# Optimization experiments

Measured on AMD Instinct MI355X. Metric: run time of the kernel, lower is better.

The kernel has to match this reference:

```python
import jax, jax.numpy as jnp
import numpy as np
import math

B, SQ, SK = 8, 1024, 1024
DQ = DK = DV = 1024
H = 16
EPS = 1e-5


def _layer_norm(x, g, b):
    mu = jnp.mean(x, axis=-1, keepdims=True)
    var = jnp.mean(jnp.square(x - mu), axis=-1, keepdims=True)
    return (x - mu) * jax.lax.rsqrt(var + EPS) * g + b


def setup_inputs() -> dict:
    key = jax.random.key(0)
    ks = jax.random.split(key, 8)
    s_q = 1.0 / math.sqrt(DQ)
    s_v = 1.0 / math.sqrt(DV)
    return {
        "Q": jax.random.normal(ks[0], (B, SQ, DQ), dtype=jnp.float32),
        "K": jax.random.normal(ks[1], (B, SK, DK), dtype=jnp.float32),
        "Wq": jax.random.normal(ks[2], (DQ, DV), dtype=jnp.float32) * s_q,
        "bq": jnp.zeros((DV,), dtype=jnp.float32),
        "Wk": jax.random.normal(ks[3], (DK, DV), dtype=jnp.float32) * s_q,
        "bk": jnp.zeros((DV,), dtype=jnp.float32),
        "Wv": jax.random.normal(ks[4], (DK, DV), dtype=jnp.float32) * s_q,
        "bv": jnp.zeros((DV,), dtype=jnp.float32),
        "Wo": jax.random.normal(ks[5], (DV, DV), dtype=jnp.float32) * s_v,
        "bo": jnp.zeros((DV,), dtype=jnp.float32),
        "g0": jnp.ones((DV,), dtype=jnp.float32),
        "b0": jnp.zeros((DV,), dtype=jnp.float32),
        "g1": jnp.ones((DV,), dtype=jnp.float32),
        "b1": jnp.zeros((DV,), dtype=jnp.float32),
    }


def reference(Q, K, Wq, bq, Wk, bk, Wv, bv, Wo, bo, g0, b0, g1, b1):
    dh = DV // H
    q = Q @ Wq + bq                      # [B,SQ,DV]
    k = K @ Wk + bk                      # [B,SK,DV]
    v = K @ Wv + bv                      # [B,SK,DV]
    # split/cat over heads == reshape to [B,S,H,dh]
    qh = q.reshape(B, SQ, H, dh)
    kh = k.reshape(B, SK, H, dh)
    vh = v.reshape(B, SK, H, dh)
    # NOTE: original scales by sqrt(dim_V), not sqrt(head_dim)
    scores = jnp.einsum("bqhd,bkhd->bhqk", qh, kh) / math.sqrt(DV)
    A = jax.nn.softmax(scores, axis=-1)  # [B,H,SQ,SK]
    attn = jnp.einsum("bhqk,bkhd->bqhd", A, vh)
    out = q + attn.reshape(B, SQ, DV)    # residual with projected Q
    out = _layer_norm(out, g0, b0)
    out = out + jax.nn.relu(out @ Wo + bo)
    out = _layer_norm(out, g1, b1)
    return out
```

## Files before the change

kernel.cpp:

```cpp
#include <hip/hip_runtime.h>
#include <hip/hip_bf16.h>
#include <stdint.h>

#define NB 8
#define NSQ 1024
#define NSK 1024
#define ND 1024
#define NH 16
#define NDH 64
#define NM (NB * NSQ)
#define LOG2E 1.4426950408889634f

typedef __bf16 bf16;
typedef __bf16 bf16x8 __attribute__((ext_vector_type(8)));
typedef float f32x4 __attribute__((ext_vector_type(4)));
typedef float f32x16 __attribute__((ext_vector_type(16)));
typedef unsigned int uint32;

__device__ __forceinline__ void async_load16(const void* g, void* l) {
  __builtin_amdgcn_global_load_lds(
      (__attribute__((address_space(1))) void*)g,
      (__attribute__((address_space(3))) void*)l, 16, 0, 0);
}

__device__ __forceinline__ void permswap(uint32& x, uint32& y) {
#if __has_builtin(__builtin_amdgcn_permlane32_swap)
  auto r = __builtin_amdgcn_permlane32_swap(x, y, false, false);
  x = r[0]; y = r[1];
#else
  asm volatile("v_permlane32_swap_b32 %0, %1" : "+v"(x), "+v"(y));
#endif
}

__global__ __launch_bounds__(256) void cvt2_f32_bf16(const float* __restrict__ A,
                                                     const float* __restrict__ B,
                                                     bf16* __restrict__ Oa,
                                                     bf16* __restrict__ Ob) {
  const float* in = blockIdx.y ? B : A;
  bf16* out = blockIdx.y ? Ob : Oa;
  int i = blockIdx.x * 256 + threadIdx.x;
  float4 v = *(const float4*)(in + (size_t)i * 4);
  union { uint64_t u; bf16 h[4]; } o;
  o.h[0] = (bf16)v.x; o.h[1] = (bf16)v.y; o.h[2] = (bf16)v.z; o.h[3] = (bf16)v.w;
  *(uint64_t*)(out + (size_t)i * 4) = o.u;
}

__global__ __launch_bounds__(256) void transpose_cvt4(
    const float* __restrict__ W0, const float* __restrict__ W1,
    const float* __restrict__ W2, const float* __restrict__ W3,
    bf16* __restrict__ O0, bf16* __restrict__ O1,
    bf16* __restrict__ O2, bf16* __restrict__ O3) {
  const float* W; bf16* Wt;
  switch (blockIdx.z) {
    case 0: W = W0; Wt = O0; break;
    case 1: W = W1; Wt = O1; break;
    case 2: W = W2; Wt = O2; break;
    default: W = W3; Wt = O3; break;
  }
  __shared__ float t[64][65];
  const int bc = blockIdx.x * 64;
  const int br = blockIdx.y * 64;
  const int tid = threadIdx.x;
  for (int c = tid; c < 1024; c += 256) {
    int r = c >> 4, off = (c & 15) * 4;
    float4 v = *(const float4*)&W[(size_t)(br + r) * 1024 + bc + off];
    t[r][off] = v.x; t[r][off + 1] = v.y; t[r][off + 2] = v.z; t[r][off + 3] = v.w;
  }
  __syncthreads();
  for (int c = tid; c < 512; c += 256) {
    int cc = c >> 3, rr = (c & 7) * 8;
    union { uint4 u; bf16 h[8]; } o;
#pragma unroll
    for (int i = 0; i < 8; ++i) o.h[i] = (bf16)t[rr + i][cc];
    *(uint4*)&Wt[(size_t)(bc + cc) * 1024 + br + rr] = o.u;
  }
}

__global__ __launch_bounds__(256) void transpose_v(const bf16* __restrict__ vsrc,
                                                   bf16* __restrict__ vT) {
  const int st = blockIdx.x * 64;
  const int bh = blockIdx.y;
  const int b = bh >> 4, h = bh & 15;
  __shared__ __align__(16) bf16 t[64][72];
  const int tid = threadIdx.x;
  for (int c = tid; c < 512; c += 256) {
    int s = c >> 3, off = (c & 7) * 8;
    *(uint4*)&t[s][off] =
        *(const uint4*)&vsrc[(size_t)(b * NSK + st + s) * 2048 + 1024 + h * NDH + off];
  }
  __syncthreads();
  for (int c = tid; c < 512; c += 256) {
    int d = c >> 3, s0 = (c & 7) * 8;
    union { uint4 u; bf16 h[8]; } o;
#pragma unroll
    for (int i = 0; i < 8; ++i) o.h[i] = t[s0 + i][d];
    *(uint4*)&vT[((size_t)(bh * NDH + d)) * NSK + st + s0] = o.u;
  }
}

template <int BM, int MODE, int NX>
__global__ __launch_bounds__(512, 2) void gemm8p(
    const bf16* __restrict__ A, const bf16* __restrict__ Bt,
    const float* __restrict__ bias, const float* __restrict__ bias2,
    bf16* __restrict__ Cb, const bf16* __restrict__ Resb, float scale, int N) {
  constexpr int RA = BM / 64;
  constexpr int NT = 16;
  constexpr int MR = BM / 32;
  __shared__ __align__(16) bf16 As[2][BM * 64];
  __shared__ __align__(16) bf16 Bs[2][256 * 64];

  const int tid = threadIdx.x;
  const int flat = blockIdx.x;
  const int nwg = gridDim.x;
  const int xi = (flat & 7) * (nwg >> 3) + (flat >> 3);
  const int bcol = (xi & (NX - 1)) * 256;
  const int brow = (xi / NX) * BM;

  const int w = tid >> 6, lane = tid & 63;
  const int wm = w >> 2, wn = w & 3;
  const int lr = lane & 15, l4 = lane >> 4;
  const int rgrp = l4 * 4;
  const int rk = lr & 7;

  const int rowoff = tid >> 3;
  const int gsrc = (tid & 7) ^ ((tid >> 3) & 7);
  const bf16* Ag = A + (size_t)(brow + rowoff) * 1024 + gsrc * 8;
  const bf16* Bg = Bt + (size_t)(bcol + rowoff) * 1024 + gsrc * 8;
  const int lds_o = rowoff * 64 + (tid & 7) * 8;

  auto stA = [&](int d, int r, int kt) {
    async_load16(Ag + (size_t)r * (64 * 1024) + kt * 64, &As[d][r * 4096 + lds_o]);
  };
  auto stB = [&](int d, int r, int kt) {
    async_load16(Bg + (size_t)r * (64 * 1024) + kt * 64, &Bs[d][r * 4096 + lds_o]);
  };
  auto fA = [&](int d, int mrow, int ks) {
    return *(const bf16x8*)&As[d][(mrow + lr) * 64 + (((ks * 4 + l4) ^ rk) * 8)];
  };
  auto fB = [&](int d, int nrow, int ks) {
    return *(const bf16x8*)&Bs[d][(nrow + lr) * 64 + (((ks * 4 + l4) ^ rk) * 8)];
  };

  f32x4 acc[MR][4] = {};
  bf16x8 af[4][2], bfr[4][2];

#pragma unroll
  for (int r = 0; r < RA; ++r) stA(0, r, 0);
#pragma unroll
  for (int r = 0; r < 4; ++r) stB(0, r, 0);
  stA(1, 0, 1);
  stA(1, 1, 1);
  asm volatile("s_waitcnt vmcnt(2)" ::: "memory");
  __builtin_amdgcn_s_barrier();

  for (int t = 0; t < NT; ++t) {
    const int cur = t & 1, nxt = cur ^ 1;
#pragma unroll
    for (int i = 0; i < 4; ++i) {
      af[i][0] = fA(cur, wm * (BM / 2) + i * 16, 0);
      af[i][1] = fA(cur, wm * (BM / 2) + i * 16, 1);
    }
#pragma unroll
    for (int j = 0; j < 2; ++j) {
      bfr[j][0] = fB(cur, wn * 64 + j * 16, 0);
      bfr[j][1] = fB(cur, wn * 64 + j * 16, 1);
    }
    if (t + 1 < NT) {
      if constexpr (BM == 256) { stA(nxt, 2, t + 1); stA(nxt, 3, t + 1); }
      else                     { stB(nxt, 0, t + 1); stB(nxt, 1, t + 1); }
    }
    __builtin_amdgcn_s_barrier();
    asm volatile("s_waitcnt lgkmcnt(0)" ::: "memory");
    __builtin_amdgcn_sched_barrier(0);
    __builtin_amdgcn_s_setprio(1);
    if constexpr (BM == 256) {
#pragma unroll
      for (int i = 0; i < 4; ++i)
#pragma unroll
        for (int j = 0; j < 2; ++j)
#pragma unroll
          for (int ks = 0; ks < 2; ++ks)
            acc[i][j] = __builtin_amdgcn_mfma_f32_16x16x32_bf16(af[i][ks], bfr[j][ks], acc[i][j], 0, 0, 0);
    } else {
#pragma unroll
      for (int i = 0; i < 4; ++i)
#pragma unroll
        for (int ks = 0; ks < 2; ++ks)
          acc[i][0] = __builtin_amdgcn_mfma_f32_16x16x32_bf16(af[i][ks], bfr[0][ks], acc[i][0], 0, 0, 0);
    }
    __builtin_amdgcn_s_setprio(0);
    __builtin_amdgcn_s_barrier();
#pragma unroll
    for (int j = 2; j < 4; ++j) {
      bfr[j][0] = fB(cur, wn * 64 + j * 16, 0);
      bfr[j][1] = fB(cur, wn * 64 + j * 16, 1);
    }
    if (t + 1 < NT) {
      if constexpr (BM == 256) { stB(nxt, 0, t + 1); stB(nxt, 1, t + 1); }
      else                     { stB(nxt, 2, t + 1); stB(nxt, 3, t + 1); }
    }
    __builtin_amdgcn_s_barrier();
    asm volatile("s_waitcnt lgkmcnt(0)" ::: "memory");
    __builtin_amdgcn_sched_barrier(0);
    __builtin_amdgcn_s_setprio(1);
    if constexpr (BM == 256) {
#pragma unroll
      for (int i = 0; i < 4; ++i)
#pragma unroll
        for (int j = 2; j < 4; ++j)
#pragma unroll
          for (int ks = 0; ks < 2; ++ks)
            acc[i][j] = __builtin_amdgcn_mfma_f32_16x16x32_bf16(af[i][ks], bfr[j][ks], acc[i][j], 0, 0, 0);
    } else {
#pragma unroll
      for (int i = 0; i < 4; ++i)
#pragma unroll
        for (int ks = 0; ks < 2; ++ks)
          acc[i][1] = __builtin_amdgcn_mfma_f32_16x16x32_bf16(af[i][ks], bfr[1][ks], acc[i][1], 0, 0, 0);
    }
    __builtin_amdgcn_s_setprio(0);
    __builtin_amdgcn_s_barrier();
    if constexpr (BM == 256) {
#pragma unroll
      for (int i = 0; i < 4; ++i) {
        af[i][0] = fA(cur, wm * 128 + 64 + i * 16, 0);
        af[i][1] = fA(cur, wm * 128 + 64 + i * 16, 1);
      }
      if (t + 1 < NT) { stB(nxt, 2, t + 1); stB(nxt, 3, t + 1); }
    }
    __builtin_amdgcn_s_barrier();
    if constexpr (BM == 256) {
      asm volatile("s_waitcnt lgkmcnt(0)" ::: "memory");
      __builtin_amdgcn_sched_barrier(0);
    }
    __builtin_amdgcn_s_setprio(1);
    if constexpr (BM == 256) {
#pragma unroll
      for (int i = 0; i < 4; ++i)
#pragma unroll
        for (int j = 0; j < 2; ++j)
#pragma unroll
          for (int ks = 0; ks < 2; ++ks)
            acc[4 + i][j] = __builtin_amdgcn_mfma_f32_16x16x32_bf16(af[i][ks], bfr[j][ks], acc[4 + i][j], 0, 0, 0);
    } else {
#pragma unroll
      for (int i = 0; i < 4; ++i)
#pragma unroll
        for (int ks = 0; ks < 2; ++ks)
          acc[i][2] = __builtin_amdgcn_mfma_f32_16x16x32_bf16(af[i][ks], bfr[2][ks], acc[i][2], 0, 0, 0);
    }
    __builtin_amdgcn_s_setprio(0);
    __builtin_amdgcn_s_barrier();
    if (t + 2 < NT) { stA(cur, 0, t + 2); stA(cur, 1, t + 2); }
    __builtin_amdgcn_s_barrier();
    __builtin_amdgcn_s_setprio(1);
    if constexpr (BM == 256) {
#pragma unroll
      for (int i = 0; i < 4; ++i)
#pragma unroll
        for (int j = 2; j < 4; ++j)
#pragma unroll
          for (int ks = 0; ks < 2; ++ks)
            acc[4 + i][j] = __builtin_amdgcn_mfma_f32_16x16x32_bf16(af[i][ks], bfr[j][ks], acc[4 + i][j], 0, 0, 0);
    } else {
#pragma unroll
      for (int i = 0; i < 4; ++i)
#pragma unroll
        for (int ks = 0; ks < 2; ++ks)
          acc[i][3] = __builtin_amdgcn_mfma_f32_16x16x32_bf16(af[i][ks], bfr[3][ks], acc[i][3], 0, 0, 0);
    }
    __builtin_amdgcn_s_setprio(0);
    if (t + 1 < NT) {
      if (t + 2 < NT) asm volatile("s_waitcnt vmcnt(2)" ::: "memory");
      else            asm volatile("s_waitcnt vmcnt(0)" ::: "memory");
    }
    __builtin_amdgcn_s_barrier();
  }

#pragma unroll
  for (int m = 0; m < MR; ++m) {
#pragma unroll
    for (int n = 0; n < 4; ++n) {
      const int col = bcol + wn * 64 + n * 16 + lr;
      float bv, sc;
      if (MODE == 2) {
        const bool isV = (bcol >= 1024);
        bv = isV ? bias2[col - 1024] : bias[col];
        sc = isV ? 1.0f : LOG2E;
      } else {
        bv = bias[col];
        sc = scale;
      }
#pragma unroll
      for (int r = 0; r < 4; ++r) {
        const int row = brow + wm * (BM / 2) + m * 16 + rgrp + r;
        float v = acc[m][n][r] + bv;
        if (MODE == 1) {
          float res = (float)Resb[(size_t)row * N + col];
          Cb[(size_t)row * N + col] = (bf16)(res + (v > 0.f ? v : 0.f));
        } else {
          Cb[(size_t)row * N + col] = (bf16)(v * sc);
        }
      }
    }
  }
}

__global__ __launch_bounds__(512, 4) void attn_kernel(
    const bf16* __restrict__ qb, const bf16* __restrict__ kvb,
    const bf16* __restrict__ vT, bf16* __restrict__ attnout) {
  const int bh = blockIdx.y;
  const int b = bh >> 4, h = bh & 15;
  const int tid = threadIdx.x, w = tid >> 6, lane = tid & 63;
  const int l31 = lane & 31;
  const int l1 = lane >> 5;
  const int q0w = blockIdx.x * 256 + w * 32;

  __shared__ __align__(16) bf16 Kl[2][64 * 64];
  __shared__ __align__(16) bf16 Vl[2][64 * 64];

  const int srow = tid >> 3;
  const int sgran = tid & 7;
  const int gsw = sgran ^ (srow & 7);
  const int ldst = srow * 64 + sgran * 8;
  const int rg = l31 & 7;

  const bf16* kbase = kvb + (size_t)(b * NSK) * 2048 + h * NDH;
  const bf16* vbase = vT + (size_t)(bh * NDH) * NSK;

  bf16x8 qf[4];
#pragma unroll
  for (int kd = 0; kd < 4; ++kd)
    qf[kd] = *(const bf16x8*)&qb[(size_t)(b * NSQ + q0w + l31) * ND +
                                 h * NDH + kd * 16 + l1 * 8];

  f32x16 oacc0 = {}, oacc1 = {}, lacc = {};
  bf16x8 ones;
#pragma unroll
  for (int i = 0; i < 8; ++i) ones[i] = (bf16)1.0f;

  auto stage = [&](int bi, int kt) {
    async_load16(kbase + (size_t)(kt + srow) * 2048 + gsw * 8, &Kl[bi][ldst]);
    async_load16(vbase + (size_t)srow * NSK + kt + gsw * 8, &Vl[bi][ldst]);
  };

  stage(0, 0);

  for (int t = 0; t < 16; ++t) {
    const int bi = t & 1;
    asm volatile("s_waitcnt vmcnt(0)" ::: "memory");
    __syncthreads();
    if (t < 15) stage(bi ^ 1, (t + 1) * 64);

    uint32 W[2][4][2];
#pragma unroll
    for (int n = 0; n < 2; ++n) {
      f32x16 s = {};
      __builtin_amdgcn_s_setprio(1);
#pragma unroll
      for (int kd = 0; kd < 4; ++kd) {
        bf16x8 kf = *(const bf16x8*)&Kl[bi][(n * 32 + l31) * 64 + (((kd * 2 + l1) ^ rg) * 8)];
        s = __builtin_amdgcn_mfma_f32_32x32x16_bf16(kf, qf[kd], s, 0, 0, 0);
      }
      __builtin_amdgcn_s_setprio(0);
#pragma unroll
      for (int r2 = 0; r2 < 4; ++r2)
#pragma unroll
        for (int p = 0; p < 2; ++p) {
          float elo = __builtin_amdgcn_exp2f(s[r2 * 4 + 2 * p]);
          float ehi = __builtin_amdgcn_exp2f(s[r2 * 4 + 2 * p + 1]);
          uint32 wd;
          asm("v_cvt_pk_bf16_f32 %0, %1, %2" : "=v"(wd) : "v"(elo), "v"(ehi));
          W[n][r2][p] = wd;
        }
    }
    __builtin_amdgcn_s_setprio(1);
#pragma unroll
    for (int kc = 0; kc < 4; ++kc) {
      uint32 x0 = W[kc >> 1][(kc & 1) * 2][0], y0 = W[kc >> 1][(kc & 1) * 2 + 1][0];
      uint32 x1 = W[kc >> 1][(kc & 1) * 2][1], y1 = W[kc >> 1][(kc & 1) * 2 + 1][1];
      permswap(x0, y0);
      permswap(x1, y1);
      union { uint32 u[4]; bf16x8 v; } cvt;
      cvt.u[0] = x0; cvt.u[1] = x1; cvt.u[2] = y0; cvt.u[3] = y1;
      bf16x8 pa = cvt.v;
      bf16x8 vf0 = *(const bf16x8*)&Vl[bi][(l31) * 64 + (((kc * 2 + l1) ^ rg) * 8)];
      bf16x8 vf1 = *(const bf16x8*)&Vl[bi][(32 + l31) * 64 + (((kc * 2 + l1) ^ rg) * 8)];
      oacc0 = __builtin_amdgcn_mfma_f32_32x32x16_bf16(pa, vf0, oacc0, 0, 0, 0);
      oacc1 = __builtin_amdgcn_mfma_f32_32x32x16_bf16(pa, vf1, oacc1, 0, 0, 0);
      lacc = __builtin_amdgcn_mfma_f32_32x32x16_bf16(pa, ones, lacc, 0, 0, 0);
    }
    __builtin_amdgcn_s_setprio(0);
  }

  float inv[16];
#pragma unroll
  for (int r = 0; r < 16; ++r) inv[r] = 1.0f / lacc[r];
#pragma unroll
  for (int r = 0; r < 16; ++r) {
    const int row = q0w + (r & 3) + 8 * (r >> 2) + 4 * l1;
    attnout[(size_t)(b * NSQ + row) * ND + h * NDH + l31] = (bf16)(oacc0[r] * inv[r]);
    attnout[(size_t)(b * NSQ + row) * ND + h * NDH + 32 + l31] = (bf16)(oacc1[r] * inv[r]);
  }
}

template <bool RES, bool OUTF>
__global__ __launch_bounds__(256) void ln_kernel(
    const bf16* __restrict__ x, const bf16* __restrict__ rq, float rscale,
    const float* __restrict__ g, const float* __restrict__ be,
    bf16* __restrict__ yb, float* __restrict__ yf) {
  __shared__ float sm[4];
  const int row = blockIdx.x, tid = threadIdx.x;
  const size_t base = (size_t)row * ND + tid * 4;
  union { uint2 u; bf16 h[4]; } xv;
  xv.u = *(const uint2*)(x + base);
  float v0 = (float)xv.h[0], v1 = (float)xv.h[1], v2 = (float)xv.h[2], v3 = (float)xv.h[3];
  if (RES) {
    union { uint2 u; bf16 h[4]; } q;
    q.u = *(const uint2*)(rq + base);
    v0 += rscale * (float)q.h[0]; v1 += rscale * (float)q.h[1];
    v2 += rscale * (float)q.h[2]; v3 += rscale * (float)q.h[3];
  }
  float s = v0 + v1 + v2 + v3;
#pragma unroll
  for (int off = 32; off > 0; off >>= 1) s += __shfl_down(s, off, 64);
  if ((tid & 63) == 0) sm[tid >> 6] = s;
  __syncthreads();
  const float mean = (sm[0] + sm[1] + sm[2] + sm[3]) * (1.0f / ND);
  __syncthreads();
  const float d0 = v0 - mean, d1 = v1 - mean, d2 = v2 - mean, d3 = v3 - mean;
  float sq = d0 * d0 + d1 * d1 + d2 * d2 + d3 * d3;
#pragma unroll
  for (int off = 32; off > 0; off >>= 1) sq += __shfl_down(sq, off, 64);
  if ((tid & 63) == 0) sm[tid >> 6] = sq;
  __syncthreads();
  const float var = (sm[0] + sm[1] + sm[2] + sm[3]) * (1.0f / ND);
  const float rs = rsqrtf(var + 1e-5f);
  float4 gv = *(const float4*)(g + tid * 4);
  float4 bv = *(const float4*)(be + tid * 4);
  const float y0 = d0 * rs * gv.x + bv.x;
  const float y1 = d1 * rs * gv.y + bv.y;
  const float y2 = d2 * rs * gv.z + bv.z;
  const float y3 = d3 * rs * gv.w + bv.w;
  if (OUTF) {
    *(float4*)(yf + base) = make_float4(y0, y1, y2, y3);
  } else {
    union { uint2 u; bf16 h[4]; } o;
    o.h[0] = (bf16)y0; o.h[1] = (bf16)y1; o.h[2] = (bf16)y2; o.h[3] = (bf16)y3;
    *(uint2*)(yb + base) = o.u;
  }
}

extern "C" void kernel_launch(void* const* d_in, const int* in_sizes, int n_in,
                              void* d_out, int out_size, void* d_ws, size_t ws_size,
                              hipStream_t stream) {
  const float* Q  = (const float*)d_in[0];
  const float* K  = (const float*)d_in[1];
  const float* Wq = (const float*)d_in[2];
  const float* bq = (const float*)d_in[3];
  const float* Wk = (const float*)d_in[4];
  const float* bk = (const float*)d_in[5];
  const float* Wv = (const float*)d_in[6];
  const float* bv = (const float*)d_in[7];
  const float* Wo = (const float*)d_in[8];
  const float* bo = (const float*)d_in[9];
  const float* g0 = (const float*)d_in[10];
  const float* b0 = (const float*)d_in[11];
  const float* g1 = (const float*)d_in[12];
  const float* b1 = (const float*)d_in[13];
  float* out = (float*)d_out;

  char* ws = (char*)d_ws;
  const size_t MB = 1024 * 1024;
  bf16* Qb    = (bf16*)(ws + 0);
  bf16* Kb    = (bf16*)(ws + 16 * MB);
  bf16* Wqt   = (bf16*)(ws + 32 * MB);
  bf16* Wkvt  = (bf16*)(ws + 34 * MB);
  bf16* Wot   = (bf16*)(ws + 38 * MB);
  bf16* qb    = (bf16*)(ws + 40 * MB);
  bf16* kvb   = (bf16*)(ws + 56 * MB);
  bf16* vT    = (bf16*)(ws + 88 * MB);
  bf16* attnb = (bf16*)(ws + 104 * MB);
  bf16* h0b   = (bf16*)(ws + 56 * MB);
  bf16* out1b = (bf16*)(ws + 0);

  cvt2_f32_bf16<<<dim3(8192, 2), 256, 0, stream>>>(Q, K, Qb, Kb);
  transpose_cvt4<<<dim3(16, 16, 4), 256, 0, stream>>>(
      Wq, Wk, Wv, Wo, Wqt, Wkvt, Wkvt + 1024 * 1024, Wot);
  gemm8p<256, 2, 8><<<256, 512, 0, stream>>>(Kb, Wkvt, bk, bv, kvb, nullptr, 1.0f, 2048);
  gemm8p<128, 0, 4><<<256, 512, 0, stream>>>(Qb, Wqt, bq, nullptr, qb, nullptr, 0.03125f, 1024);
  transpose_v<<<dim3(16, 128), 256, 0, stream>>>(kvb, vT);
  attn_kernel<<<dim3(4, 128), 512, 0, stream>>>(qb, kvb, vT, attnb);
  ln_kernel<true, false><<<8192, 256, 0, stream>>>(attnb, qb, 32.0f, g0, b0, h0b, nullptr);
  gemm8p<128, 1, 4><<<256, 512, 0, stream>>>(h0b, Wot, bo, nullptr, out1b, h0b, 1.0f, 1024);
  ln_kernel<false, true><<<8192, 256, 0, stream>>>(out1b, nullptr, 0.f, g1, b1, nullptr, out);
}
```

Before: 182.1 us.

## Replace 8-wave double-buffered GEMM with 4-wave triple-buffered K=32 pipeline

Rewrites the projection GEMM kernel to use 256-thread workgroups with 128-wide column tiles and a K step of 32, staged through a three-deep LDS ring buffer instead of the previous two-phase double buffer with interleaved partial loads. Each iteration loads fragments, issues the async load two tiles ahead, runs one MFMA block and syncs once. This is meant to simplify scheduling, reduce barriers per K step and double the grid size for better CU occupancy. The trade-offs are smaller tiles with less data reuse per workgroup, twice as many loop iterations, and a different LDS swizzle.

```diff
diff --git a/kernel.cpp b/kernel.cpp
--- a/kernel.cpp
+++ b/kernel.cpp
@@ -98,183 +98,79 @@
   }
 }
 
-template <int BM, int MODE, int NX>
-__global__ __launch_bounds__(512, 2) void gemm8p(
+template <int BM, int MODE, int NXC>
+__global__ __launch_bounds__(256, 2) void gemm3b(
     const bf16* __restrict__ A, const bf16* __restrict__ Bt,
     const float* __restrict__ bias, const float* __restrict__ bias2,
     bf16* __restrict__ Cb, const bf16* __restrict__ Resb, float scale, int N) {
-  constexpr int RA = BM / 64;
-  constexpr int NT = 16;
+  constexpr int NT = 32;
+  constexpr int AR = BM / 64;
   constexpr int MR = BM / 32;
-  __shared__ __align__(16) bf16 As[2][BM * 64];
-  __shared__ __align__(16) bf16 Bs[2][256 * 64];
+  __shared__ __align__(16) bf16 Asl[3][BM * 32];
+  __shared__ __align__(16) bf16 Bsl[3][128 * 32];
 
   const int tid = threadIdx.x;
   const int flat = blockIdx.x;
-  const int nwg = gridDim.x;
-  const int xi = (flat & 7) * (nwg >> 3) + (flat >> 3);
-  const int bcol = (xi & (NX - 1)) * 256;
-  const int brow = (xi / NX) * BM;
+  const int xi = (flat & 7) * 64 + (flat >> 3);
+  const int bcol = (xi & (NXC - 1)) * 128;
+  const int brow = (xi / NXC) * BM;
 
   const int w = tid >> 6, lane = tid & 63;
-  const int wm = w >> 2, wn = w & 3;
+  const int wm = w >> 1, wn = w & 1;
   const int lr = lane & 15, l4 = lane >> 4;
   const int rgrp = l4 * 4;
-  const int rk = lr & 7;
-
-  const int rowoff = tid >> 3;
-  const int gsrc = (tid & 7) ^ ((tid >> 3) & 7);
-  const bf16* Ag = A + (size_t)(brow + rowoff) * 1024 + gsrc * 8;
-  const bf16* Bg = Bt + (size_t)(bcol + rowoff) * 1024 + gsrc * 8;
-  const int lds_o = rowoff * 64 + (tid & 7) * 8;
-
-  auto stA = [&](int d, int r, int kt) {
-    async_load16(Ag + (size_t)r * (64 * 1024) + kt * 64, &As[d][r * 4096 + lds_o]);
+  const int gph = (l4 ^ ((lr >> 1) & 3)) * 8;
+
+  const int srow = tid >> 2;
+  const int gsrc = (tid & 3) ^ ((tid >> 3) & 3);
+  const bf16* Ag = A + (size_t)(brow + srow) * 1024 + gsrc * 8;
+  const bf16* Bg = Bt + (size_t)(bcol + srow) * 1024 + gsrc * 8;
+  const int ldo = srow * 32 + (tid & 3) * 8;
+
+  auto stage = [&](int d, int kt) {
+#pragma unroll
+    for (int r = 0; r < AR; ++r)
+      async_load16(Ag + (size_t)r * (64 * 1024) + kt * 32, &Asl[d][r * 2048 + ldo]);
+#pragma unroll
+    for (int r = 0; r < 2; ++r)
+      async_load16(Bg + (size_t)r * (64 * 1024) + kt * 32, &Bsl[d][r * 2048 + ldo]);
   };
-  auto stB = [&](int d, int r, int kt) {
-    async_load16(Bg + (size_t)r * (64 * 1024) + kt * 64, &Bs[d][r * 4096 + lds_o]);
+  auto wait_tile = [&]() {
+    if constexpr (BM == 256) asm volatile("s_waitcnt vmcnt(6)" ::: "memory");
+    else                     asm volatile("s_waitcnt vmcnt(4)" ::: "memory");
   };
-  auto fA = [&](int d, int mrow, int ks) {
-    return *(const bf16x8*)&As[d][(mrow + lr) * 64 + (((ks * 4 + l4) ^ rk) * 8)];
-  };
-  auto fB = [&](int d, int nrow, int ks) {
-    return *(const bf16x8*)&Bs[d][(nrow + lr) * 64 + (((ks * 4 + l4) ^ rk) * 8)];
-  };
 
   f32x4 acc[MR][4] = {};
-  bf16x8 af[4][2], bfr[4][2];
-
-#pragma unroll
-  for (int r = 0; r < RA; ++r) stA(0, r, 0);
-#pragma unroll
-  for (int r = 0; r < 4; ++r) stB(0, r, 0);
-  stA(1, 0, 1);
-  stA(1, 1, 1);
-  asm volatile("s_waitcnt vmcnt(2)" ::: "memory");
+
+  stage(0, 0);
+  stage(1, 1);
+  wait_tile();
   __builtin_amdgcn_s_barrier();
 
+  int cur = 0, st2 = 2;
   for (int t = 0; t < NT; ++t) {
-    const int cur = t & 1, nxt = cur ^ 1;
-#pragma unroll
-    for (int i = 0; i < 4; ++i) {
-      af[i][0] = fA(cur, wm * (BM / 2) + i * 16, 0);
-      af[i][1] = fA(cur, wm * (BM / 2) + i * 16, 1);
-    }
-#pragma unroll
-    for (int j = 0; j < 2; ++j) {
-      bfr[j][0] = fB(cur, wn * 64 + j * 16, 0);
-      bfr[j][1] = fB(cur, wn * 64 + j * 16, 1);
-    }
-    if (t + 1 < NT) {
-      if constexpr (BM == 256) { stA(nxt, 2, t + 1); stA(nxt, 3, t + 1); }
-      else                     { stB(nxt, 0, t + 1); stB(nxt, 1, t + 1); }
-    }
-    __builtin_amdgcn_s_barrier();
+    bf16x8 af[MR], bfr[4];
+#pragma unroll
+    for (int i = 0; i < MR; ++i)
+      af[i] = *(const bf16x8*)&Asl[cur][(wm * (BM / 2) + i * 16 + lr) * 32 + gph];
+#pragma unroll
+    for (int n = 0; n < 4; ++n)
+      bfr[n] = *(const bf16x8*)&Bsl[cur][(wn * 64 + n * 16 + lr) * 32 + gph];
+    if (t + 2 < NT) stage(st2, t + 2);
     asm volatile("s_waitcnt lgkmcnt(0)" ::: "memory");
     __builtin_amdgcn_sched_barrier(0);
     __builtin_amdgcn_s_setprio(1);
-    if constexpr (BM == 256) {
-#pragma unroll
-      for (int i = 0; i < 4; ++i)
-#pragma unroll
-        for (int j = 0; j < 2; ++j)
-#pragma unroll
-          for (int ks = 0; ks < 2; ++ks)
-            acc[i][j] = __builtin_amdgcn_mfma_f32_16x16x32_bf16(af[i][ks], bfr[j][ks], acc[i][j], 0, 0, 0);
-    } else {
-#pragma unroll
-      for (int i = 0; i < 4; ++i)
-#pragma unroll
-        for (int ks = 0; ks < 2; ++ks)
-          acc[i][0] = __builtin_amdgcn_mfma_f32_16x16x32_bf16(af[i][ks], bfr[0][ks], acc[i][0], 0, 0, 0);
-    }
+#pragma unroll
+    for (int i = 0; i < MR; ++i)
+#pragma unroll
+      for (int n = 0; n < 4; ++n)
+        acc[i][n] = __builtin_amdgcn_mfma_f32_16x16x32_bf16(af[i], bfr[n], acc[i][n], 0, 0, 0);
     __builtin_amdgcn_s_setprio(0);
+    if (t + 2 < NT)      wait_tile();
+    else if (t + 1 < NT) asm volatile("s_waitcnt vmcnt(0)" ::: "memory");
     __builtin_amdgcn_s_barrier();
-#pragma unroll
-    for (int j = 2; j < 4; ++j) {
-      bfr[j][0] = fB(cur, wn * 64 + j * 16, 0);
-      bfr[j][1] = fB(cur, wn * 64 + j * 16, 1);
-    }
-    if (t + 1 < NT) {
-      if constexpr (BM == 256) { stB(nxt, 0, t + 1); stB(nxt, 1, t + 1); }
-      else                     { stB(nxt, 2, t + 1); stB(nxt, 3, t + 1); }
-    }
-    __builtin_amdgcn_s_barrier();
-    asm volatile("s_waitcnt lgkmcnt(0)" ::: "memory");
-    __builtin_amdgcn_sched_barrier(0);
-    __builtin_amdgcn_s_setprio(1);
-    if constexpr (BM == 256) {
-#pragma unroll
-      for (int i = 0; i < 4; ++i)
-#pragma unroll
-        for (int j = 2; j < 4; ++j)
-#pragma unroll
-          for (int ks = 0; ks < 2; ++ks)
-            acc[i][j] = __builtin_amdgcn_mfma_f32_16x16x32_bf16(af[i][ks], bfr[j][ks], acc[i][j], 0, 0, 0);
-    } else {
-#pragma unroll
-      for (int i = 0; i < 4; ++i)
-#pragma unroll
-        for (int ks = 0; ks < 2; ++ks)
-          acc[i][1] = __builtin_amdgcn_mfma_f32_16x16x32_bf16(af[i][ks], bfr[1][ks], acc[i][1], 0, 0, 0);
-    }
-    __builtin_amdgcn_s_setprio(0);
-    __builtin_amdgcn_s_barrier();
-    if constexpr (BM == 256) {
-#pragma unroll
-      for (int i = 0; i < 4; ++i) {
-        af[i][0] = fA(cur, wm * 128 + 64 + i * 16, 0);
-        af[i][1] = fA(cur, wm * 128 + 64 + i * 16, 1);
-      }
-      if (t + 1 < NT) { stB(nxt, 2, t + 1); stB(nxt, 3, t + 1); }
-    }
-    __builtin_amdgcn_s_barrier();
-    if constexpr (BM == 256) {
-      asm volatile("s_waitcnt lgkmcnt(0)" ::: "memory");
-      __builtin_amdgcn_sched_barrier(0);
-    }
-    __builtin_amdgcn_s_setprio(1);
-    if constexpr (BM == 256) {
-#pragma unroll
-      for (int i = 0; i < 4; ++i)
-#pragma unroll
-        for (int j = 0; j < 2; ++j)
-#pragma unroll
-          for (int ks = 0; ks < 2; ++ks)
-            acc[4 + i][j] = __builtin_amdgcn_mfma_f32_16x16x32_bf16(af[i][ks], bfr[j][ks], acc[4 + i][j], 0, 0, 0);
-    } else {
-#pragma unroll
-      for (int i = 0; i < 4; ++i)
-#pragma unroll
-        for (int ks = 0; ks < 2; ++ks)
-          acc[i][2] = __builtin_amdgcn_mfma_f32_16x16x32_bf16(af[i][ks], bfr[2][ks], acc[i][2], 0, 0, 0);
-    }
-    __builtin_amdgcn_s_setprio(0);
-    __builtin_amdgcn_s_barrier();
-    if (t + 2 < NT) { stA(cur, 0, t + 2); stA(cur, 1, t + 2); }
-    __builtin_amdgcn_s_barrier();
-    __builtin_amdgcn_s_setprio(1);
-    if constexpr (BM == 256) {
-#pragma unroll
-      for (int i = 0; i < 4; ++i)
-#pragma unroll
-        for (int j = 2; j < 4; ++j)
-#pragma unroll
-          for (int ks = 0; ks < 2; ++ks)
-            acc[4 + i][j] = __builtin_amdgcn_mfma_f32_16x16x32_bf16(af[i][ks], bfr[j][ks], acc[4 + i][j], 0, 0, 0);
-    } else {
-#pragma unroll
-      for (int i = 0; i < 4; ++i)
-#pragma unroll
-        for (int ks = 0; ks < 2; ++ks)
-          acc[i][3] = __builtin_amdgcn_mfma_f32_16x16x32_bf16(af[i][ks], bfr[3][ks], acc[i][3], 0, 0, 0);
-    }
-    __builtin_amdgcn_s_setprio(0);
-    if (t + 1 < NT) {
-      if (t + 2 < NT) asm volatile("s_waitcnt vmcnt(2)" ::: "memory");
-      else            asm volatile("s_waitcnt vmcnt(0)" ::: "memory");
-    }
-    __builtin_amdgcn_s_barrier();
+    cur = (cur == 2) ? 0 : cur + 1;
+    st2 = (st2 == 2) ? 0 : st2 + 1;
   }
 
 #pragma unroll
@@ -487,11 +383,11 @@
   cvt2_f32_bf16<<<dim3(8192, 2), 256, 0, stream>>>(Q, K, Qb, Kb);
   transpose_cvt4<<<dim3(16, 16, 4), 256, 0, stream>>>(
       Wq, Wk, Wv, Wo, Wqt, Wkvt, Wkvt + 1024 * 1024, Wot);
-  gemm8p<256, 2, 8><<<256, 512, 0, stream>>>(Kb, Wkvt, bk, bv, kvb, nullptr, 1.0f, 2048);
-  gemm8p<128, 0, 4><<<256, 512, 0, stream>>>(Qb, Wqt, bq, nullptr, qb, nullptr, 0.03125f, 1024);
+  gemm3b<256, 2, 16><<<512, 256, 0, stream>>>(Kb, Wkvt, bk, bv, kvb, nullptr, 1.0f, 2048);
+  gemm3b<128, 0, 8><<<512, 256, 0, stream>>>(Qb, Wqt, bq, nullptr, qb, nullptr, 0.03125f, 1024);
   transpose_v<<<dim3(16, 128), 256, 0, stream>>>(kvb, vT);
   attn_kernel<<<dim3(4, 128), 512, 0, stream>>>(qb, kvb, vT, attnb);
   ln_kernel<true, false><<<8192, 256, 0, stream>>>(attnb, qb, 32.0f, g0, b0, h0b, nullptr);
-  gemm8p<128, 1, 4><<<256, 512, 0, stream>>>(h0b, Wot, bo, nullptr, out1b, h0b, 1.0f, 1024);
+  gemm3b<128, 1, 8><<<512, 256, 0, stream>>>(h0b, Wot, bo, nullptr, out1b, h0b, 1.0f, 1024);
   ln_kernel<false, true><<<8192, 256, 0, stream>>>(out1b, nullptr, 0.f, g1, b1, nullptr, out);
 }
```

After: 180.1 us. No clear change (-1.1%).
